# Kernel tuning notes

Hardware: AMD Instinct MI355X
Metric: run time of the kernel (lower is better)

The kernel has to match this reference:

```python
import jax, jax.numpy as jnp
import numpy as np

N_GRAPHS = 64
ATOMS = 32
N = N_GRAPHS * ATOMS          # 2048 total nodes
HID = 128                     # num_hidden_feature
FEAT = 64                     # num_ligand_atom_feature
D1_MIN, D1_MAX, D1_BINS = 0.0, 10.0, 32   # dist_one_hot_param1
D2_BINS = 64                  # dist_one_hot_param2[-1]
N_DENSE = 3
GAMMA = 10.0                  # SoftOneHot gaussian width
NEG = -9e15


def _linear_init(key, n_out, n_in):
    kw, kb = jax.random.split(key)
    bound = 1.0 / np.sqrt(n_in)
    W = jax.random.uniform(kw, (n_out, n_in), jnp.float32, -bound, bound)
    b = jax.random.uniform(kb, (n_out,), jnp.float32, -bound, bound)
    return W, b


def setup_inputs() -> dict:
    key = jax.random.key(0)
    ks = jax.random.split(key, 12)
    h = jax.random.normal(ks[0], (N, HID), jnp.float32)
    pos = jax.random.normal(ks[1], (N, 3), jnp.float32) * 3.0
    next_type = jax.random.normal(ks[2], (N_GRAPHS, FEAT), jnp.float32)
    batch = (jnp.arange(N, dtype=jnp.int32) // ATOMS)  # sorted segment ids

    W_emb = _linear_init(ks[3], HID, FEAT)[0]          # embedding has no bias
    W_qkv, b_qkv = _linear_init(ks[4], 3 * HID, HID)
    W_b, b_b = _linear_init(ks[5], 1, HID)
    W_g, b_g = _linear_init(ks[6], 1, HID)
    W_t, b_t = _linear_init(ks[7], 1, D1_BINS)
    dims = list(np.linspace(HID, D2_BINS, N_DENSE + 1).astype(int))  # [128,106,85,64]
    W_d0, b_d0 = _linear_init(ks[8], dims[1], dims[0])
    W_d1, b_d1 = _linear_init(ks[9], dims[2], dims[1])
    W_d2, b_d2 = _linear_init(ks[10], dims[3], dims[2])
    return {"h": h, "pos": pos, "next_type": next_type, "batch": batch,
            "W_emb": W_emb, "W_qkv": W_qkv, "b_qkv": b_qkv,
            "W_b": W_b, "b_b": b_b, "W_g": W_g, "b_g": b_g,
            "W_t": W_t, "b_t": b_t,
            "W_d0": W_d0, "b_d0": b_d0, "W_d1": W_d1, "b_d1": b_d1,
            "W_d2": W_d2, "b_d2": b_d2}


def reference(h, pos, next_type, batch, W_emb, W_qkv, b_qkv, W_b, b_b,
              W_g, b_g, W_t, b_t, W_d0, b_d0, W_d1, b_d1, W_d2, b_d2):
    # length per graph (scatter_add of ones)
    length = jax.ops.segment_sum(jnp.ones((N,), jnp.float32), batch,
                                 num_segments=N_GRAPHS)
    # dist_embed = h * embedding(next_type)[batch]
    x = h * (next_type @ W_emb.T)[batch]

    sqrt_len = (length ** -0.5)[batch]                 # [N]
    # block-diagonal mask (batch is sorted, so equality == block diag)
    mask = batch[:, None] == batch[None, :]            # [N,N] bool

    # cdist + SoftOneHot (gaussian soft one-hot over linspace centers)
    sq = jnp.sum((pos[:, None, :] - pos[None, :, :]) ** 2, -1)
    d = jnp.sqrt(jnp.maximum(sq, 1e-12))               # [N,N]
    centers = jnp.linspace(D1_MIN, D1_MAX, D1_BINS)
    intra = jnp.exp(-GAMMA * (d[..., None] - centers) ** 2)  # [N,N,BINS]
    t = jnp.einsum('ijk,k->ij', intra, W_t[0]) + b_t[0]      # t_proj.squeeze(-1)

    qkv = x @ W_qkv.T + b_qkv
    q, k, v = jnp.split(qkv, 3, axis=-1)
    b_bias = x @ W_b.T + b_b                           # [N,1], per-row bias
    g = jax.nn.sigmoid(x @ W_g.T + b_g)                # [N,1] gate

    logits = (q @ k.T) * sqrt_len[:, None] + b_bias + t
    logits = jnp.where(mask, logits, NEG)
    attn = jax.nn.softmax(logits, axis=-1)
    vals = (attn @ v) * g + x                          # gated residual

    # dense head: SiLU between layers, none after last
    y = jax.nn.silu(vals @ W_d0.T + b_d0)
    y = jax.nn.silu(y @ W_d1.T + b_d1)
    y = y @ W_d2.T + b_d2
    return jax.nn.log_softmax(y, axis=-1)
```

## Files before the change

### kernel.cpp

```cpp
#include <hip/hip_runtime.h>

typedef __bf16 bf16_t;
typedef __bf16 bf16x8 __attribute__((ext_vector_type(8)));
typedef float  f32x4  __attribute__((ext_vector_type(4)));

#define HPAD   132
#define LDSPAD 136
#define VPAD   40

__device__ __forceinline__ bf16x8 zero8() {
    bf16x8 v;
#pragma unroll
    for (int i = 0; i < 8; ++i) v[i] = (bf16_t)0.0f;
    return v;
}

__device__ __forceinline__ bf16x8 cvt8(const float* __restrict__ p) {
    bf16x8 v;
#pragma unroll
    for (int i = 0; i < 8; ++i) v[i] = (bf16_t)p[i];
    return v;
}

__global__ __launch_bounds__(256)
void nextdist_fused(const float* __restrict__ h,
                    const float* __restrict__ pos,
                    const float* __restrict__ ntype,
                    const float* __restrict__ Wemb,
                    const float* __restrict__ Wqkv,
                    const float* __restrict__ bqkv,
                    const float* __restrict__ Wg,
                    const float* __restrict__ bg,
                    const float* __restrict__ Wt,
                    const float* __restrict__ bt,
                    const float* __restrict__ Wd0, const float* __restrict__ bd0,
                    const float* __restrict__ Wd1, const float* __restrict__ bd1,
                    const float* __restrict__ Wd2, const float* __restrict__ bd2,
                    float* __restrict__ out)
{
    __shared__ __align__(16) float  s_hf[32 * HPAD];
    __shared__ __align__(16) bf16_t s_x [32 * LDSPAD];
    __shared__ __align__(16) bf16_t s_q [32 * LDSPAD];
    __shared__ __align__(16) bf16_t s_k [32 * LDSPAD];
    __shared__ __align__(16) bf16_t s_vT[128 * VPAD];
    __shared__ __align__(16) bf16_t s_p [32 * VPAD];
    __shared__ __align__(16) float  s_t [32 * 33];
    __shared__ __align__(16) float  s_y2[32 * 66];
    __shared__ float s_emb[128];
    __shared__ float s_nt[64];
    __shared__ float s_pos[96];
    __shared__ float s_wt[32];
    __shared__ float s_wg[128];
    __shared__ float s_gate[32];

    const int tid  = threadIdx.x;
    const int wave = tid >> 6;
    const int lane = tid & 63;
    const int quad = lane >> 4;
    const int l16  = lane & 15;
    const int g    = blockIdx.x;
    const int base = g * 32;

    for (int c = tid; c < 1024; c += 256) {
        int a = c >> 5, ch = c & 31;
        *(float4*)&s_hf[a * HPAD + ch * 4] = *(const float4*)&h[(base + a) * 128 + ch * 4];
    }
    if (tid < 96)  s_pos[tid] = pos[base * 3 + tid];
    if (tid < 64)  s_nt[tid]  = ntype[g * 64 + tid];
    if (tid < 32)  s_wt[tid]  = Wt[tid];
    if (tid < 128) s_wg[tid]  = Wg[tid];
    __syncthreads();

    if (tid < 128) {
        float acc = 0.0f;
#pragma unroll 8
        for (int f = 0; f < 64; ++f) acc += Wemb[tid * 64 + f] * s_nt[f];
        s_emb[tid] = acc;
    }
    __syncthreads();

    for (int c = tid; c < 4096; c += 256) {
        int a = c >> 7, f = c & 127;
        s_x[a * LDSPAD + f] = (bf16_t)(s_hf[a * HPAD + f] * s_emb[f]);
    }
    if (tid < 32) {
        float acc = 0.0f;
#pragma unroll 8
        for (int f = 0; f < 128; ++f) acc += s_hf[tid * HPAD + f] * s_emb[f] * s_wg[f];
        acc += bg[0];
        s_gate[tid] = 1.0f / (1.0f + __expf(-acc));
    }
    __syncthreads();

    for (int nti = 0; nti < 6; ++nti) {
        int nt = wave + nti * 4;
        int o  = nt * 16 + l16;
        const float* wrow = &Wqkv[o * 128];
        for (int mt = 0; mt < 2; ++mt) {
            f32x4 acc = {0.f, 0.f, 0.f, 0.f};
#pragma unroll
            for (int ks = 0; ks < 4; ++ks) {
                bf16x8 av = *(const bf16x8*)&s_x[(mt * 16 + l16) * LDSPAD + ks * 32 + quad * 8];
                bf16x8 bv = cvt8(&wrow[ks * 32 + quad * 8]);
                acc = __builtin_amdgcn_mfma_f32_16x16x32_bf16(av, bv, acc, 0, 0, 0);
            }
            float bias = bqkv[o];
#pragma unroll
            for (int r = 0; r < 4; ++r) {
                int a = mt * 16 + quad * 4 + r;
                float val = acc[r] + bias;
                if (o < 128)      s_q[a * LDSPAD + o]         = (bf16_t)val;
                else if (o < 256) s_k[a * LDSPAD + (o - 128)] = (bf16_t)val;
                else              s_vT[(o - 256) * VPAD + a]  = (bf16_t)val;
            }
        }
    }

    {
        const float bt0 = bt[0];
        for (int e = tid; e < 1024; e += 256) {
            int i = e >> 5, j = e & 31;
            float dx = s_pos[i * 3 + 0] - s_pos[j * 3 + 0];
            float dy = s_pos[i * 3 + 1] - s_pos[j * 3 + 1];
            float dz = s_pos[i * 3 + 2] - s_pos[j * 3 + 2];
            float d  = sqrtf(fmaxf(dx * dx + dy * dy + dz * dz, 1e-12f));
            float acc = bt0;
#pragma unroll
            for (int kk = 0; kk < 32; ++kk) {
                float u = d - (float)kk * (10.0f / 31.0f);
                acc += s_wt[kk] * __expf(-10.0f * u * u);
            }
            s_t[i * 33 + j] = acc;
        }
    }
    __syncthreads();

    {
        int mt = wave >> 1, nt = wave & 1;
        f32x4 acc = {0.f, 0.f, 0.f, 0.f};
#pragma unroll
        for (int ks = 0; ks < 4; ++ks) {
            bf16x8 av = *(const bf16x8*)&s_q[(mt * 16 + l16) * LDSPAD + ks * 32 + quad * 8];
            bf16x8 bv = *(const bf16x8*)&s_k[(nt * 16 + l16) * LDSPAD + ks * 32 + quad * 8];
            acc = __builtin_amdgcn_mfma_f32_16x16x32_bf16(av, bv, acc, 0, 0, 0);
        }
#pragma unroll
        for (int r = 0; r < 4; ++r) {
            int i = mt * 16 + quad * 4 + r, j = nt * 16 + l16;
            s_t[i * 33 + j] = acc[r] * 0.17677669529663687f + s_t[i * 33 + j];
        }
    }
    __syncthreads();

    {
        int r = tid >> 3, sub = tid & 7;
        float v[4]; float mx = -1e30f;
#pragma unroll
        for (int c = 0; c < 4; ++c) { v[c] = s_t[r * 33 + sub * 4 + c]; mx = fmaxf(mx, v[c]); }
#pragma unroll
        for (int s = 1; s < 8; s <<= 1) mx = fmaxf(mx, __shfl_xor(mx, s, 64));
        float sum = 0.0f;
#pragma unroll
        for (int c = 0; c < 4; ++c) { v[c] = __expf(v[c] - mx); sum += v[c]; }
#pragma unroll
        for (int s = 1; s < 8; s <<= 1) sum += __shfl_xor(sum, s, 64);
        float inv = 1.0f / sum;
#pragma unroll
        for (int c = 0; c < 4; ++c) s_p[r * VPAD + sub * 4 + c] = (bf16_t)(v[c] * inv);
    }
    __syncthreads();

#pragma unroll
    for (int nn = 0; nn < 2; ++nn) {
        int nt = wave + nn * 4;
#pragma unroll
        for (int mt = 0; mt < 2; ++mt) {
            bf16x8 av = *(const bf16x8*)&s_p[(mt * 16 + l16) * VPAD + quad * 8];
            bf16x8 bv = *(const bf16x8*)&s_vT[(nt * 16 + l16) * VPAD + quad * 8];
            f32x4 acc = {0.f, 0.f, 0.f, 0.f};
            acc = __builtin_amdgcn_mfma_f32_16x16x32_bf16(av, bv, acc, 0, 0, 0);
#pragma unroll
            for (int r = 0; r < 4; ++r) {
                int a = mt * 16 + quad * 4 + r, f = nt * 16 + l16;
                float val = acc[r] * s_gate[a] + s_hf[a * HPAD + f] * s_emb[f];
                s_x[a * LDSPAD + f] = (bf16_t)val;
            }
        }
    }
    __syncthreads();

    for (int e = tid; e < 32 * 16; e += 256) {
        int a = e >> 4, c = 112 + (e & 15);
        s_q[a * LDSPAD + c] = (bf16_t)0.0f;
    }
    for (int t8 = 0; t8 < 2; ++t8) {
        int nt = wave + t8 * 4;
        if (nt < 7) {
            int o = nt * 16 + l16;
            bool ov = o < 106;
            const float* wrow = &Wd0[o * 128];
            for (int mt = 0; mt < 2; ++mt) {
                f32x4 acc = {0.f, 0.f, 0.f, 0.f};
#pragma unroll
                for (int ks = 0; ks < 4; ++ks) {
                    bf16x8 av = *(const bf16x8*)&s_x[(mt * 16 + l16) * LDSPAD + ks * 32 + quad * 8];
                    bf16x8 bv = ov ? cvt8(&wrow[ks * 32 + quad * 8]) : zero8();
                    acc = __builtin_amdgcn_mfma_f32_16x16x32_bf16(av, bv, acc, 0, 0, 0);
                }
                float bias = ov ? bd0[o] : 0.0f;
#pragma unroll
                for (int r = 0; r < 4; ++r) {
                    int a = mt * 16 + quad * 4 + r;
                    float val = acc[r] + bias;
                    float y = val / (1.0f + __expf(-val));
                    s_q[a * LDSPAD + o] = ov ? (bf16_t)y : (bf16_t)0.0f;
                }
            }
        }
    }
    __syncthreads();

    for (int t8 = 0; t8 < 2; ++t8) {
        int nt = wave + t8 * 4;
        if (nt < 6) {
            int o = nt * 16 + l16;
            bool ov = o < 85;
            const float* wrow = &Wd1[o * 106];
            for (int mt = 0; mt < 2; ++mt) {
                f32x4 acc = {0.f, 0.f, 0.f, 0.f};
#pragma unroll
                for (int ks = 0; ks < 4; ++ks) {
                    int kb = ks * 32 + quad * 8;
                    bf16x8 av = *(const bf16x8*)&s_q[(mt * 16 + l16) * LDSPAD + kb];
                    bf16x8 bv;
#pragma unroll
                    for (int jj = 0; jj < 8; ++jj) {
                        int k = kb + jj;
                        bv[jj] = (ov && k < 106) ? (bf16_t)wrow[k] : (bf16_t)0.0f;
                    }
                    acc = __builtin_amdgcn_mfma_f32_16x16x32_bf16(av, bv, acc, 0, 0, 0);
                }
                float bias = ov ? bd1[o] : 0.0f;
#pragma unroll
                for (int r = 0; r < 4; ++r) {
                    int a = mt * 16 + quad * 4 + r;
                    float val = acc[r] + bias;
                    float y = val / (1.0f + __expf(-val));
                    s_k[a * LDSPAD + o] = ov ? (bf16_t)y : (bf16_t)0.0f;
                }
            }
        }
    }
    __syncthreads();

    {
        int nt = wave;
        int o  = nt * 16 + l16;
        const float* wrow = &Wd2[o * 85];
        for (int mt = 0; mt < 2; ++mt) {
            f32x4 acc = {0.f, 0.f, 0.f, 0.f};
#pragma unroll
            for (int ks = 0; ks < 3; ++ks) {
                int kb = ks * 32 + quad * 8;
                bf16x8 av = *(const bf16x8*)&s_k[(mt * 16 + l16) * LDSPAD + kb];
                bf16x8 bv;
#pragma unroll
                for (int jj = 0; jj < 8; ++jj) {
                    int k = kb + jj;
                    bv[jj] = (k < 85) ? (bf16_t)wrow[k] : (bf16_t)0.0f;
                }
                acc = __builtin_amdgcn_mfma_f32_16x16x32_bf16(av, bv, acc, 0, 0, 0);
            }
            float bias = bd2[o];
#pragma unroll
            for (int r = 0; r < 4; ++r) {
                int a = mt * 16 + quad * 4 + r;
                s_y2[a * 66 + o] = acc[r] + bias;
            }
        }
    }
    __syncthreads();

    {
        int r = tid >> 3, sub = tid & 7;
        float v[8]; float mx = -1e30f;
#pragma unroll
        for (int c = 0; c < 8; ++c) { v[c] = s_y2[r * 66 + sub * 8 + c]; mx = fmaxf(mx, v[c]); }
#pragma unroll
        for (int s = 1; s < 8; s <<= 1) mx = fmaxf(mx, __shfl_xor(mx, s, 64));
        float sum = 0.0f;
#pragma unroll
        for (int c = 0; c < 8; ++c) sum += __expf(v[c] - mx);
#pragma unroll
        for (int s = 1; s < 8; s <<= 1) sum += __shfl_xor(sum, s, 64);
        float lse = mx + __logf(sum);
#pragma unroll
        for (int c = 0; c < 8; ++c)
            out[(base + r) * 64 + sub * 8 + c] = v[c] - lse;
    }
}

extern "C" void kernel_launch(void* const* d_in, const int* in_sizes, int n_in,
                              void* d_out, int out_size, void* d_ws, size_t ws_size,
                              hipStream_t stream) {
    const float* h     = (const float*)d_in[0];
    const float* pos   = (const float*)d_in[1];
    const float* ntype = (const float*)d_in[2];
    const float* Wemb  = (const float*)d_in[4];
    const float* Wqkv  = (const float*)d_in[5];
    const float* bqkv  = (const float*)d_in[6];
    const float* Wg    = (const float*)d_in[9];
    const float* bg    = (const float*)d_in[10];
    const float* Wt    = (const float*)d_in[11];
    const float* bt    = (const float*)d_in[12];
    const float* Wd0   = (const float*)d_in[13];
    const float* bd0   = (const float*)d_in[14];
    const float* Wd1   = (const float*)d_in[15];
    const float* bd1   = (const float*)d_in[16];
    const float* Wd2   = (const float*)d_in[17];
    const float* bd2   = (const float*)d_in[18];
    float* out = (float*)d_out;

    nextdist_fused<<<dim3(64), dim3(256), 0, stream>>>(
        h, pos, ntype, Wemb, Wqkv, bqkv, Wg, bg, Wt, bt,
        Wd0, bd0, Wd1, bd1, Wd2, bd2, out);
}
```

Baseline: 127.9 us.

## Preconvert weights to padded bf16 and widen fused kernel to 1024 threads

Adds a separate kernel that converts the QKV and dense-head weights to bf16 with zero-padding, written into a workspace, so the main kernel can load weight fragments with vector loads instead of per-element fp32 conversion and bounds checks. The fused kernel grows from 256 to 1024 threads per block, and work is redistributed so each wave handles a single MFMA tile. The embedding and gate dot products become shuffle reductions, and the distance-embedding loop gives one element per thread. In exchange it adds a second kernel launch each call, and with only 64 blocks many waves sit idle in the smaller phases.

```diff
diff --git a/kernel.cpp b/kernel.cpp
--- a/kernel.cpp
+++ b/kernel.cpp
@@ -8,34 +8,46 @@
 #define LDSPAD 136
 #define VPAD   40
 
-__device__ __forceinline__ bf16x8 zero8() {
-    bf16x8 v;
-#pragma unroll
-    for (int i = 0; i < 8; ++i) v[i] = (bf16_t)0.0f;
-    return v;
+#define WQ_OFF   0
+#define WD0_OFF  49152
+#define WD1_OFF  63488
+#define WD2_OFF  75776
+#define WS_ELEMS 81920
+
+__global__ __launch_bounds__(256)
+void preconvert(const float* __restrict__ Wqkv, const float* __restrict__ Wd0,
+                const float* __restrict__ Wd1, const float* __restrict__ Wd2,
+                bf16_t* __restrict__ ws) {
+    int i = blockIdx.x * 256 + threadIdx.x;
+    if (i >= WS_ELEMS) return;
+    if (i < WD0_OFF) {
+        ws[i] = (bf16_t)Wqkv[i];
+    } else if (i < WD1_OFF) {
+        int j = i - WD0_OFF, r = j >> 7, c = j & 127;
+        ws[i] = (r < 106) ? (bf16_t)Wd0[r * 128 + c] : (bf16_t)0.0f;
+    } else if (i < WD2_OFF) {
+        int j = i - WD1_OFF, r = j >> 7, c = j & 127;
+        ws[i] = (r < 85 && c < 106) ? (bf16_t)Wd1[r * 106 + c] : (bf16_t)0.0f;
+    } else {
+        int j = i - WD2_OFF, r = j / 96, c = j - r * 96;
+        ws[i] = (c < 85) ? (bf16_t)Wd2[r * 85 + c] : (bf16_t)0.0f;
+    }
 }
 
-__device__ __forceinline__ bf16x8 cvt8(const float* __restrict__ p) {
-    bf16x8 v;
-#pragma unroll
-    for (int i = 0; i < 8; ++i) v[i] = (bf16_t)p[i];
-    return v;
-}
-
-__global__ __launch_bounds__(256)
+__global__ __launch_bounds__(1024)
 void nextdist_fused(const float* __restrict__ h,
                     const float* __restrict__ pos,
                     const float* __restrict__ ntype,
                     const float* __restrict__ Wemb,
-                    const float* __restrict__ Wqkv,
                     const float* __restrict__ bqkv,
                     const float* __restrict__ Wg,
                     const float* __restrict__ bg,
                     const float* __restrict__ Wt,
                     const float* __restrict__ bt,
-                    const float* __restrict__ Wd0, const float* __restrict__ bd0,
-                    const float* __restrict__ Wd1, const float* __restrict__ bd1,
-                    const float* __restrict__ Wd2, const float* __restrict__ bd2,
+                    const float* __restrict__ bd0,
+                    const float* __restrict__ bd1,
+                    const float* __restrict__ bd2,
+                    const bf16_t* __restrict__ ws,
                     float* __restrict__ out)
 {
     __shared__ __align__(16) float  s_hf[32 * HPAD];
@@ -53,6 +65,11 @@
     __shared__ float s_wg[128];
     __shared__ float s_gate[32];
 
+    const bf16_t* __restrict__ Wqkvb = ws + WQ_OFF;
+    const bf16_t* __restrict__ Wd0b  = ws + WD0_OFF;
+    const bf16_t* __restrict__ Wd1b  = ws + WD1_OFF;
+    const bf16_t* __restrict__ Wd2b  = ws + WD2_OFF;
+
     const int tid  = threadIdx.x;
     const int wave = tid >> 6;
     const int lane = tid & 63;
@@ -61,8 +78,8 @@
     const int g    = blockIdx.x;
     const int base = g * 32;
 
-    for (int c = tid; c < 1024; c += 256) {
-        int a = c >> 5, ch = c & 31;
+    {
+        int a = tid >> 5, ch = tid & 31;
         *(float4*)&s_hf[a * HPAD + ch * 4] = *(const float4*)&h[(base + a) * 128 + ch * 4];
     }
     if (tid < 96)  s_pos[tid] = pos[base * 3 + tid];
@@ -71,71 +88,72 @@
     if (tid < 128) s_wg[tid]  = Wg[tid];
     __syncthreads();
 
-    if (tid < 128) {
+    {
+        int o = tid >> 3, p = tid & 7;
         float acc = 0.0f;
-#pragma unroll 8
-        for (int f = 0; f < 64; ++f) acc += Wemb[tid * 64 + f] * s_nt[f];
-        s_emb[tid] = acc;
-    }
-    __syncthreads();
-
-    for (int c = tid; c < 4096; c += 256) {
+#pragma unroll
+        for (int f = p * 8; f < p * 8 + 8; ++f) acc += Wemb[o * 64 + f] * s_nt[f];
+#pragma unroll
+        for (int s = 1; s < 8; s <<= 1) acc += __shfl_xor(acc, s, 64);
+        if (p == 0) s_emb[o] = acc;
+    }
+    __syncthreads();
+
+    for (int c = tid; c < 4096; c += 1024) {
         int a = c >> 7, f = c & 127;
         s_x[a * LDSPAD + f] = (bf16_t)(s_hf[a * HPAD + f] * s_emb[f]);
     }
-    if (tid < 32) {
+    if (tid < 256) {
+        int r = tid >> 3, p = tid & 7;
         float acc = 0.0f;
-#pragma unroll 8
-        for (int f = 0; f < 128; ++f) acc += s_hf[tid * HPAD + f] * s_emb[f] * s_wg[f];
-        acc += bg[0];
-        s_gate[tid] = 1.0f / (1.0f + __expf(-acc));
-    }
-    __syncthreads();
-
-    for (int nti = 0; nti < 6; ++nti) {
-        int nt = wave + nti * 4;
+#pragma unroll
+        for (int f = p * 16; f < p * 16 + 16; ++f) acc += s_hf[r * HPAD + f] * s_emb[f] * s_wg[f];
+#pragma unroll
+        for (int s = 1; s < 8; s <<= 1) acc += __shfl_xor(acc, s, 64);
+        if (p == 0) s_gate[r] = 1.0f / (1.0f + __expf(-(acc + bg[0])));
+    }
+    __syncthreads();
+
+    for (int t = wave; t < 48; t += 16) {
+        int nt = t >> 1, mt = t & 1;
         int o  = nt * 16 + l16;
-        const float* wrow = &Wqkv[o * 128];
-        for (int mt = 0; mt < 2; ++mt) {
-            f32x4 acc = {0.f, 0.f, 0.f, 0.f};
-#pragma unroll
-            for (int ks = 0; ks < 4; ++ks) {
-                bf16x8 av = *(const bf16x8*)&s_x[(mt * 16 + l16) * LDSPAD + ks * 32 + quad * 8];
-                bf16x8 bv = cvt8(&wrow[ks * 32 + quad * 8]);
-                acc = __builtin_amdgcn_mfma_f32_16x16x32_bf16(av, bv, acc, 0, 0, 0);
-            }
-            float bias = bqkv[o];
-#pragma unroll
-            for (int r = 0; r < 4; ++r) {
-                int a = mt * 16 + quad * 4 + r;
-                float val = acc[r] + bias;
-                if (o < 128)      s_q[a * LDSPAD + o]         = (bf16_t)val;
-                else if (o < 256) s_k[a * LDSPAD + (o - 128)] = (bf16_t)val;
-                else              s_vT[(o - 256) * VPAD + a]  = (bf16_t)val;
-            }
+        const bf16_t* wrow = &Wqkvb[o * 128];
+        f32x4 acc = {0.f, 0.f, 0.f, 0.f};
+#pragma unroll
+        for (int ks = 0; ks < 4; ++ks) {
+            bf16x8 av = *(const bf16x8*)&s_x[(mt * 16 + l16) * LDSPAD + ks * 32 + quad * 8];
+            bf16x8 bv = *(const bf16x8*)&wrow[ks * 32 + quad * 8];
+            acc = __builtin_amdgcn_mfma_f32_16x16x32_bf16(av, bv, acc, 0, 0, 0);
+        }
+        float bias = bqkv[o];
+#pragma unroll
+        for (int r = 0; r < 4; ++r) {
+            int a = mt * 16 + quad * 4 + r;
+            float val = acc[r] + bias;
+            if (o < 128)      s_q[a * LDSPAD + o]         = (bf16_t)val;
+            else if (o < 256) s_k[a * LDSPAD + (o - 128)] = (bf16_t)val;
+            else              s_vT[(o - 256) * VPAD + a]  = (bf16_t)val;
         }
     }
 
     {
         const float bt0 = bt[0];
-        for (int e = tid; e < 1024; e += 256) {
-            int i = e >> 5, j = e & 31;
-            float dx = s_pos[i * 3 + 0] - s_pos[j * 3 + 0];
-            float dy = s_pos[i * 3 + 1] - s_pos[j * 3 + 1];
-            float dz = s_pos[i * 3 + 2] - s_pos[j * 3 + 2];
-            float d  = sqrtf(fmaxf(dx * dx + dy * dy + dz * dz, 1e-12f));
-            float acc = bt0;
-#pragma unroll
-            for (int kk = 0; kk < 32; ++kk) {
-                float u = d - (float)kk * (10.0f / 31.0f);
-                acc += s_wt[kk] * __expf(-10.0f * u * u);
-            }
-            s_t[i * 33 + j] = acc;
-        }
-    }
-    __syncthreads();
-
-    {
+        int i = tid >> 5, j = tid & 31;
+        float dx = s_pos[i * 3 + 0] - s_pos[j * 3 + 0];
+        float dy = s_pos[i * 3 + 1] - s_pos[j * 3 + 1];
+        float dz = s_pos[i * 3 + 2] - s_pos[j * 3 + 2];
+        float d  = sqrtf(fmaxf(dx * dx + dy * dy + dz * dz, 1e-12f));
+        float acc = bt0;
+#pragma unroll
+        for (int kk = 0; kk < 32; ++kk) {
+            float u = d - (float)kk * (10.0f / 31.0f);
+            acc += s_wt[kk] * __expf(-10.0f * u * u);
+        }
+        s_t[i * 33 + j] = acc;
+    }
+    __syncthreads();
+
+    if (wave < 4) {
         int mt = wave >> 1, nt = wave & 1;
         f32x4 acc = {0.f, 0.f, 0.f, 0.f};
 #pragma unroll
@@ -152,7 +170,7 @@
     }
     __syncthreads();
 
-    {
+    if (tid < 256) {
         int r = tid >> 3, sub = tid & 7;
         float v[4]; float mx = -1e30f;
 #pragma unroll
@@ -170,118 +188,88 @@
     }
     __syncthreads();
 
-#pragma unroll
-    for (int nn = 0; nn < 2; ++nn) {
-        int nt = wave + nn * 4;
-#pragma unroll
-        for (int mt = 0; mt < 2; ++mt) {
-            bf16x8 av = *(const bf16x8*)&s_p[(mt * 16 + l16) * VPAD + quad * 8];
-            bf16x8 bv = *(const bf16x8*)&s_vT[(nt * 16 + l16) * VPAD + quad * 8];
-            f32x4 acc = {0.f, 0.f, 0.f, 0.f};
-            acc = __builtin_amdgcn_mfma_f32_16x16x32_bf16(av, bv, acc, 0, 0, 0);
-#pragma unroll
-            for (int r = 0; r < 4; ++r) {
-                int a = mt * 16 + quad * 4 + r, f = nt * 16 + l16;
-                float val = acc[r] * s_gate[a] + s_hf[a * HPAD + f] * s_emb[f];
-                s_x[a * LDSPAD + f] = (bf16_t)val;
-            }
-        }
-    }
-    __syncthreads();
-
-    for (int e = tid; e < 32 * 16; e += 256) {
-        int a = e >> 4, c = 112 + (e & 15);
+    {
+        int nt = wave >> 1, mt = wave & 1;
+        bf16x8 av = *(const bf16x8*)&s_p[(mt * 16 + l16) * VPAD + quad * 8];
+        bf16x8 bv = *(const bf16x8*)&s_vT[(nt * 16 + l16) * VPAD + quad * 8];
+        f32x4 acc = {0.f, 0.f, 0.f, 0.f};
+        acc = __builtin_amdgcn_mfma_f32_16x16x32_bf16(av, bv, acc, 0, 0, 0);
+#pragma unroll
+        for (int r = 0; r < 4; ++r) {
+            int a = mt * 16 + quad * 4 + r, f = nt * 16 + l16;
+            float val = acc[r] * s_gate[a] + s_hf[a * HPAD + f] * s_emb[f];
+            s_x[a * LDSPAD + f] = (bf16_t)val;
+        }
+    }
+    if (tid < 512) {
+        int a = tid >> 4, c = 112 + (tid & 15);
         s_q[a * LDSPAD + c] = (bf16_t)0.0f;
     }
-    for (int t8 = 0; t8 < 2; ++t8) {
-        int nt = wave + t8 * 4;
-        if (nt < 7) {
-            int o = nt * 16 + l16;
-            bool ov = o < 106;
-            const float* wrow = &Wd0[o * 128];
-            for (int mt = 0; mt < 2; ++mt) {
-                f32x4 acc = {0.f, 0.f, 0.f, 0.f};
-#pragma unroll
-                for (int ks = 0; ks < 4; ++ks) {
-                    bf16x8 av = *(const bf16x8*)&s_x[(mt * 16 + l16) * LDSPAD + ks * 32 + quad * 8];
-                    bf16x8 bv = ov ? cvt8(&wrow[ks * 32 + quad * 8]) : zero8();
-                    acc = __builtin_amdgcn_mfma_f32_16x16x32_bf16(av, bv, acc, 0, 0, 0);
-                }
-                float bias = ov ? bd0[o] : 0.0f;
-#pragma unroll
-                for (int r = 0; r < 4; ++r) {
-                    int a = mt * 16 + quad * 4 + r;
-                    float val = acc[r] + bias;
-                    float y = val / (1.0f + __expf(-val));
-                    s_q[a * LDSPAD + o] = ov ? (bf16_t)y : (bf16_t)0.0f;
-                }
-            }
-        }
-    }
-    __syncthreads();
-
-    for (int t8 = 0; t8 < 2; ++t8) {
-        int nt = wave + t8 * 4;
-        if (nt < 6) {
-            int o = nt * 16 + l16;
-            bool ov = o < 85;
-            const float* wrow = &Wd1[o * 106];
-            for (int mt = 0; mt < 2; ++mt) {
-                f32x4 acc = {0.f, 0.f, 0.f, 0.f};
-#pragma unroll
-                for (int ks = 0; ks < 4; ++ks) {
-                    int kb = ks * 32 + quad * 8;
-                    bf16x8 av = *(const bf16x8*)&s_q[(mt * 16 + l16) * LDSPAD + kb];
-                    bf16x8 bv;
-#pragma unroll
-                    for (int jj = 0; jj < 8; ++jj) {
-                        int k = kb + jj;
-                        bv[jj] = (ov && k < 106) ? (bf16_t)wrow[k] : (bf16_t)0.0f;
-                    }
-                    acc = __builtin_amdgcn_mfma_f32_16x16x32_bf16(av, bv, acc, 0, 0, 0);
-                }
-                float bias = ov ? bd1[o] : 0.0f;
-#pragma unroll
-                for (int r = 0; r < 4; ++r) {
-                    int a = mt * 16 + quad * 4 + r;
-                    float val = acc[r] + bias;
-                    float y = val / (1.0f + __expf(-val));
-                    s_k[a * LDSPAD + o] = ov ? (bf16_t)y : (bf16_t)0.0f;
-                }
-            }
-        }
-    }
-    __syncthreads();
-
-    {
-        int nt = wave;
-        int o  = nt * 16 + l16;
-        const float* wrow = &Wd2[o * 85];
-        for (int mt = 0; mt < 2; ++mt) {
-            f32x4 acc = {0.f, 0.f, 0.f, 0.f};
-#pragma unroll
-            for (int ks = 0; ks < 3; ++ks) {
-                int kb = ks * 32 + quad * 8;
-                bf16x8 av = *(const bf16x8*)&s_k[(mt * 16 + l16) * LDSPAD + kb];
-                bf16x8 bv;
-#pragma unroll
-                for (int jj = 0; jj < 8; ++jj) {
-                    int k = kb + jj;
-                    bv[jj] = (k < 85) ? (bf16_t)wrow[k] : (bf16_t)0.0f;
-                }
-                acc = __builtin_amdgcn_mfma_f32_16x16x32_bf16(av, bv, acc, 0, 0, 0);
-            }
-            float bias = bd2[o];
-#pragma unroll
-            for (int r = 0; r < 4; ++r) {
-                int a = mt * 16 + quad * 4 + r;
-                s_y2[a * 66 + o] = acc[r] + bias;
-            }
-        }
-    }
-    __syncthreads();
-
-    {
+    __syncthreads();
+
+    if (wave < 14) {
+        int nt = wave >> 1, mt = wave & 1;
+        int o = nt * 16 + l16;
+        const bf16_t* wrow = &Wd0b[o * 128];
+        f32x4 acc = {0.f, 0.f, 0.f, 0.f};
+#pragma unroll
+        for (int ks = 0; ks < 4; ++ks) {
+            bf16x8 av = *(const bf16x8*)&s_x[(mt * 16 + l16) * LDSPAD + ks * 32 + quad * 8];
+            bf16x8 bv = *(const bf16x8*)&wrow[ks * 32 + quad * 8];
+            acc = __builtin_amdgcn_mfma_f32_16x16x32_bf16(av, bv, acc, 0, 0, 0);
+        }
+        float bias = (o < 106) ? bd0[o] : 0.0f;
+#pragma unroll
+        for (int r = 0; r < 4; ++r) {
+            int a = mt * 16 + quad * 4 + r;
+            float val = acc[r] + bias;
+            s_q[a * LDSPAD + o] = (bf16_t)(val / (1.0f + __expf(-val)));
+        }
+    }
+    __syncthreads();
+
+    if (wave < 12) {
+        int nt = wave >> 1, mt = wave & 1;
+        int o = nt * 16 + l16;
+        const bf16_t* wrow = &Wd1b[o * 128];
+        f32x4 acc = {0.f, 0.f, 0.f, 0.f};
+#pragma unroll
+        for (int ks = 0; ks < 4; ++ks) {
+            bf16x8 av = *(const bf16x8*)&s_q[(mt * 16 + l16) * LDSPAD + ks * 32 + quad * 8];
+            bf16x8 bv = *(const bf16x8*)&wrow[ks * 32 + quad * 8];
+            acc = __builtin_amdgcn_mfma_f32_16x16x32_bf16(av, bv, acc, 0, 0, 0);
+        }
+        float bias = (o < 85) ? bd1[o] : 0.0f;
+#pragma unroll
+        for (int r = 0; r < 4; ++r) {
+            int a = mt * 16 + quad * 4 + r;
+            float val = acc[r] + bias;
+            s_k[a * LDSPAD + o] = (bf16_t)(val / (1.0f + __expf(-val)));
+        }
+    }
+    __syncthreads();
+
+    if (wave < 8) {
+        int nt = wave >> 1, mt = wave & 1;
+        int o = nt * 16 + l16;
+        const bf16_t* wrow = &Wd2b[o * 96];
+        f32x4 acc = {0.f, 0.f, 0.f, 0.f};
+#pragma unroll
+        for (int ks = 0; ks < 3; ++ks) {
+            bf16x8 av = *(const bf16x8*)&s_k[(mt * 16 + l16) * LDSPAD + ks * 32 + quad * 8];
+            bf16x8 bv = *(const bf16x8*)&wrow[ks * 32 + quad * 8];
+            acc = __builtin_amdgcn_mfma_f32_16x16x32_bf16(av, bv, acc, 0, 0, 0);
+        }
+        float bias = bd2[o];
+#pragma unroll
+        for (int r = 0; r < 4; ++r) {
+            int a = mt * 16 + quad * 4 + r;
+            s_y2[a * 66 + o] = acc[r] + bias;
+        }
+    }
+    __syncthreads();
+
+    if (tid < 256) {
         int r = tid >> 3, sub = tid & 7;
         float v[8]; float mx = -1e30f;
 #pragma unroll
@@ -320,8 +308,10 @@
     const float* Wd2   = (const float*)d_in[17];
     const float* bd2   = (const float*)d_in[18];
     float* out = (float*)d_out;
-
-    nextdist_fused<<<dim3(64), dim3(256), 0, stream>>>(
-        h, pos, ntype, Wemb, Wqkv, bqkv, Wg, bg, Wt, bt,
-        Wd0, bd0, Wd1, bd1, Wd2, bd2, out);
+    bf16_t* ws = (bf16_t*)d_ws;
+
+    preconvert<<<dim3((WS_ELEMS + 255) / 256), dim3(256), 0, stream>>>(Wqkv, Wd0, Wd1, Wd2, ws);
+    nextdist_fused<<<dim3(64), dim3(1024), 0, stream>>>(
+        h, pos, ntype, Wemb, bqkv, Wg, bg, Wt, bt,
+        bd0, bd1, bd2, ws, out);
 }
```

Measured after the change: 109.4 us. -14.5%, faster.
